# Performance work log

Measured on AMD Instinct MI355X. Metric: run time of the kernel, lower is better.

## Reference

```python
import jax, jax.numpy as jnp
import numpy as np

N = 50000        # n nodes (cells)
C = 1024         # common genes
H = 128          # edge_h_dim
HG = 128         # edge_hidden
E = 1600000      # edges (avg degree 32)
LAYERS = 2       # gnn_layers (unset in original __init__; fixed here)
EPS = 1e-8


def setup_inputs() -> dict:
    key = jax.random.key(0)
    ks = jax.random.split(key, 10)
    x_common = jax.random.normal(ks[0], (N, C), dtype=jnp.float32)
    src = jax.random.randint(ks[1], (E,), 0, N, dtype=jnp.int32)
    dst = jax.random.randint(ks[2], (E,), 0, N, dtype=jnp.int32)
    base_w = jax.random.uniform(ks[3], (E,), dtype=jnp.float32)
    # encoder params: Linear(C,H) -> ReLU -> Linear(H,H) -> ReLU
    W1 = jax.random.normal(ks[4], (C, H), dtype=jnp.float32) * 0.02
    b1 = jnp.zeros((H,), dtype=jnp.float32)
    W2 = jax.random.normal(ks[5], (H, H), dtype=jnp.float32) * 0.1
    b2 = jnp.zeros((H,), dtype=jnp.float32)
    # edge gate params: Linear(2H, HG) -> ReLU -> Linear(HG, 1)
    Wg1 = jax.random.normal(ks[6], (2 * H, HG), dtype=jnp.float32) * 0.1
    bg1 = jnp.zeros((HG,), dtype=jnp.float32)
    Wg2 = jax.random.normal(ks[7], (HG, 1), dtype=jnp.float32) * 0.1
    bg2 = jnp.full((1,), 2.0, dtype=jnp.float32)  # original init: bias=2.0
    # node reliability logits
    rho_raw = jax.random.normal(ks[8], (N,), dtype=jnp.float32) * 0.5
    return dict(x_common=x_common, src=src, dst=dst, base_w=base_w,
                W1=W1, b1=b1, W2=W2, b2=b2,
                Wg1=Wg1, bg1=bg1, Wg2=Wg2, bg2=bg2, rho_raw=rho_raw)


def reference(x_common, src, dst, base_w, W1, b1, W2, b2, Wg1, bg1, Wg2, bg2, rho_raw):
    # enc: [N, C] -> [N, H]
    h = jax.nn.relu(jax.nn.relu(x_common @ W1 + b1) @ W2 + b2)
    rho = jax.nn.sigmoid(rho_raw)                 # [N]
    rr = rho[src] * rho[dst]                      # [E] per-edge reliability factor
    for _ in range(LAYERS):
        h_src = h[src]                            # [E, H] gather
        h_dst = h[dst]                            # [E, H] gather
        z = jnp.concatenate([h_src, h_dst], axis=1)               # [E, 2H]
        gate = jax.nn.sigmoid(jax.nn.relu(z @ Wg1 + bg1) @ Wg2 + bg2)[:, 0]  # [E]
        w = base_w * gate * rr                    # [E]
        m = jax.ops.segment_sum(w[:, None] * h_src, dst, num_segments=N)     # [N, H]
        deg = jax.ops.segment_sum(w, dst, num_segments=N)                    # [N]
        h = m / (deg[:, None] + EPS)
    return h
```

## Files before the change

### kernel.cpp

```cpp
#include <hip/hip_runtime.h>
#include <stdint.h>

#define NN 50000
#define CC 1024
#define HH 128
#define EE 1600000
#define EPSV 1e-8f
#define NSTRIPE 8
#define STRIPE_N 6250
#define NBUCK (NN*NSTRIPE)
#define SCAN_BLKS 1563

typedef __attribute__((ext_vector_type(8))) short bf16x8;
typedef __attribute__((ext_vector_type(4))) float f32x4;
typedef __attribute__((ext_vector_type(2))) float f32x2;

__device__ __forceinline__ unsigned short f32_to_bf16(float f){
  union { float f; uint32_t u; } cv; cv.f = f;
  uint32_t u = cv.u;
  return (unsigned short)((u + 0x7FFFu + ((u >> 16) & 1u)) >> 16);
}
__device__ __forceinline__ float bf16lo_to_f32(uint32_t w){
  union { uint32_t u; float f; } cv; cv.u = w << 16; return cv.f;
}
__device__ __forceinline__ float bf16hi_to_f32(uint32_t w){
  union { uint32_t u; float f; } cv; cv.u = w & 0xFFFF0000u; return cv.f;
}

#define DPP_ADD(x, ctrl) ((x) + __int_as_float(__builtin_amdgcn_update_dpp(0, __float_as_int(x), (ctrl), 0xF, 0xF, true)))

#define GLOAD_LDS16(g, l) __builtin_amdgcn_global_load_lds( \
    (const __attribute__((address_space(1))) uint32_t*)(g), \
    (__attribute__((address_space(3))) uint32_t*)(l), 16, 0, 0)


__global__ __launch_bounds__(256) void k_prep_all(
    const float* __restrict__ W1, const float* __restrict__ W2,
    const float* __restrict__ Wg1,
    unsigned short* __restrict__ W1T, unsigned short* __restrict__ W2T,
    unsigned short* __restrict__ Wg1T){
  int idx = blockIdx.x*256 + threadIdx.x;
  if(idx < 131072){
    int n = idx >> 10, k = idx & 1023;
    W1T[idx] = f32_to_bf16(W1[k*128 + n]);
  } else if(idx < 131072 + 16384){
    int i = idx - 131072;
    int n = i >> 7, k = i & 127;
    W2T[i] = f32_to_bf16(W2[k*128 + n]);
  } else if(idx < 131072 + 16384 + 32768){
    int i = idx - 131072 - 16384;
    int c = i >> 7, k = i & 127;
    int row = (c < 128) ? k : (128 + k);
    int col = (c < 128) ? c : (c - 128);
    Wg1T[i] = f32_to_bf16(Wg1[row*128 + col]);
  }
}


__global__ __launch_bounds__(256) void k_hist(const int* __restrict__ src,
    const int* __restrict__ dst, int* __restrict__ counts,
    int* __restrict__ rank){
  int e = blockIdx.x*256 + threadIdx.x;
  if(e >= EE) return;
  int key = dst[e]*NSTRIPE + (int)((unsigned)src[e] / STRIPE_N);
  rank[e] = atomicAdd(&counts[key], 1);
}

__global__ __launch_bounds__(256) void k_scan1(const int* __restrict__ counts,
    int* __restrict__ lexcl, int* __restrict__ bsum){
  __shared__ int buf[256];
  const int t = threadIdx.x, i = blockIdx.x*256 + t;
  int v = (i < NBUCK) ? counts[i] : 0;
  buf[t] = v;
  __syncthreads();
  for(int off = 1; off < 256; off <<= 1){
    int add = (t >= off) ? buf[t-off] : 0;
    __syncthreads();
    buf[t] += add;
    __syncthreads();
  }
  if(i < NBUCK) lexcl[i] = buf[t] - v;
  if(t == 255) bsum[blockIdx.x] = buf[255];
}

__global__ __launch_bounds__(1024) void k_scan_mid(const int* __restrict__ bsum,
    int* __restrict__ bexcl){
  __shared__ int buf[1024];
  __shared__ int carry_s;
  const int t = threadIdx.x;
  if(t == 0) carry_s = 0;
  __syncthreads();
  for(int base = 0; base < SCAN_BLKS; base += 1024){
    int v = (base+t < SCAN_BLKS) ? bsum[base+t] : 0;
    buf[t] = v;
    __syncthreads();
    for(int off = 1; off < 1024; off <<= 1){
      int add = (t >= off) ? buf[t-off] : 0;
      __syncthreads();
      buf[t] += add;
      __syncthreads();
    }
    int carry = carry_s;
    if(base+t < SCAN_BLKS) bexcl[base+t] = carry + buf[t] - v;
    __syncthreads();
    if(t == 1023) carry_s = carry + buf[1023];
    __syncthreads();
  }
}

__global__ __launch_bounds__(256) void k_scan3(const int* __restrict__ lexcl,
    const int* __restrict__ bexcl, int* __restrict__ bptr){
  const int i = blockIdx.x*256 + threadIdx.x;
  if(i < NBUCK) bptr[i] = lexcl[i] + bexcl[blockIdx.x];
  if(i == 0) bptr[NBUCK] = EE;
}

__global__ __launch_bounds__(256) void k_fill(const int* __restrict__ src,
    const int* __restrict__ dst, const float* __restrict__ base_w,
    const float* __restrict__ rho_raw, const int* __restrict__ bptr,
    const int* __restrict__ rank, float2* __restrict__ scp){
  int e = blockIdx.x*256 + threadIdx.x;
  if(e >= EE) return;
  int s = src[e], d = dst[e];
  int key = d*NSTRIPE + (int)((unsigned)s / STRIPE_N);
  int p = bptr[key] + rank[e];
  float rs = 1.f/(1.f + __expf(-rho_raw[s]));
  float rd = 1.f/(1.f + __expf(-rho_raw[d]));
  scp[p] = make_float2(base_w[e]*rs*rd, __int_as_float(s));
}


__global__ __launch_bounds__(256) void k_enc1(
    const float* __restrict__ X, const unsigned short* __restrict__ W1T,
    const float* __restrict__ b1, unsigned short* __restrict__ h1)
{
  __shared__ __attribute__((aligned(16))) float          Af[3][32*32];
  __shared__ __attribute__((aligned(16))) unsigned short Bf[3][128*32];

  const int t = threadIdx.x, w = t >> 6, lane = t & 63;
  const int rowL = lane & 15, kq = lane >> 4;
  const int wm = w >> 1, wn = w & 1;
  const int row0 = blockIdx.x * 32;

  const int a_rl = w*8 + (lane >> 3);
  const int a_cl = lane & 7;
  int agr = row0 + a_rl; if(agr >= NN) agr = NN-1;
  const float* a_src = X + (size_t)agr*1024 + (a_cl ^ (a_rl & 7))*4;
  const int b_rl0 = w*32 + (lane >> 2);
  const int b_cl  = lane & 3;
  const int bkey0 = (b_rl0 ^ (b_rl0 >> 2)) & 3;
  const int bkey1 = ((b_rl0+16) ^ ((b_rl0+16) >> 2)) & 3;
  const unsigned short* b_src0 = W1T + (size_t)b_rl0*1024 + (b_cl ^ bkey0)*8;
  const unsigned short* b_src1 = W1T + (size_t)(b_rl0+16)*1024 + (b_cl ^ bkey1)*8;

  #define STAGE(buf, k0)  do{                                              \
    GLOAD_LDS16(a_src  + (k0), &Af[buf][(w*8)*32]);                        \
    GLOAD_LDS16(b_src0 + (k0), &Bf[buf][(w*32     )*32]);                  \
    GLOAD_LDS16(b_src1 + (k0), &Bf[buf][(w*32 + 16)*32]);                  \
  }while(0)

  f32x4 acc[4] = {};
  const int arow  = wm*16 + rowL;
  const int akey  = rowL & 7;
  const int bkeyR = (rowL ^ (rowL >> 2)) & 3;

  auto COMPUTE = [&](const float* afb, const unsigned short* bfb){
    f32x4 x0 = *(const f32x4*)&afb[arow*32 + (((2*kq  ) ^ akey) << 2)];
    f32x4 x1 = *(const f32x4*)&afb[arow*32 + (((2*kq+1) ^ akey) << 2)];
    union { bf16x8 v; unsigned short s[8]; } pk;
    #pragma unroll
    for(int j = 0; j < 4; j++){ pk.s[j] = f32_to_bf16(x0[j]); pk.s[4+j] = f32_to_bf16(x1[j]); }
    bf16x8 bfr[4];
    #pragma unroll
    for(int nf = 0; nf < 4; nf++){
      const int br = wn*64 + nf*16 + rowL;
      bfr[nf] = *(const bf16x8*)&bfb[br*32 + ((kq ^ bkeyR) << 3)];
    }
    #pragma unroll
    for(int nf = 0; nf < 4; nf++)
      acc[nf] = __builtin_amdgcn_mfma_f32_16x16x32_bf16(pk.v, bfr[nf], acc[nf], 0, 0, 0);
  };

  #define STEP(cbuf, sbuf, sk, vN)  do{                                    \
    if((sk) >= 0) STAGE(sbuf, (sk)*32);                                    \
    asm volatile("s_waitcnt vmcnt(" #vN ")" ::: "memory");                 \
    __builtin_amdgcn_s_barrier();                                          \
    __builtin_amdgcn_sched_barrier(0);                                     \
    COMPUTE(&Af[cbuf][0], &Bf[cbuf][0]);                                   \
    __builtin_amdgcn_s_barrier();                                          \
  }while(0)

  STAGE(0, 0);
  STAGE(1, 32);

  for(int tt = 0; tt < 30; tt += 3){
    STEP(0, 2, tt + 2, 6);
    STEP(1, 0, tt + 3, 6);
    STEP(2, 1, tt + 4, 6);
  }
  STEP(0, 0, -1, 3);
  asm volatile("s_waitcnt vmcnt(0)" ::: "memory");
  __builtin_amdgcn_s_barrier();
  __builtin_amdgcn_sched_barrier(0);
  COMPUTE(&Af[1][0], &Bf[1][0]);
  #undef STEP
  #undef STAGE

  #pragma unroll
  for(int nf = 0; nf < 4; nf++){
    const int col = wn*64 + nf*16 + rowL;
    const float bv = b1[col];
    #pragma unroll
    for(int r = 0; r < 4; r++){
      const int gr = row0 + wm*16 + kq*4 + r;
      if(gr < NN) h1[(size_t)gr*128 + col] = f32_to_bf16(fmaxf(acc[nf][r] + bv, 0.f));
    }
  }
}


__device__ __forceinline__ void uv_phase2(
    const unsigned short* hs, const unsigned short* wgl, int row0, int wave, int lane,
    const float* __restrict__ bg1,
    unsigned short* __restrict__ UH, float* __restrict__ Vf)
{
  const int rowL = lane & 15, kq = lane >> 4;
  const int r = wave*16 + rowL;
  f32x4 acc[16] = {};
  #pragma unroll
  for(int ks = 0; ks < 4; ks++){
    const int kc = ks*4 + kq;
    bf16x8 a = *(const bf16x8*)&hs[r*128 + ((kc ^ (r & 15)) << 3)];
    #pragma unroll
    for(int nt = 0; nt < 16; nt++){
      bf16x8 b = *(const bf16x8*)&wgl[(nt*16 + rowL)*128 + ((kc ^ rowL) << 3)];
      acc[nt] = __builtin_amdgcn_mfma_f32_16x16x32_bf16(a, b, acc[nt], 0, 0, 0);
    }
  }
  #pragma unroll
  for(int nt = 0; nt < 16; nt++){
    const int col = nt*16 + rowL;
    #pragma unroll
    for(int rr = 0; rr < 4; rr++){
      const int gr = row0 + wave*16 + kq*4 + rr;
      if(gr < NN){
        if(col < 128) UH[(size_t)gr*256 + col] = f32_to_bf16(acc[nt][rr]);
        else          Vf[(size_t)gr*128 + col - 128] = acc[nt][rr] + bg1[col - 128];
      }
    }
  }
}


__global__ __launch_bounds__(256) void k_uvA(
    const unsigned short* __restrict__ h1, const unsigned short* __restrict__ W2T,
    const float* __restrict__ b2, const unsigned short* __restrict__ Wg1T,
    const float* __restrict__ bg1, unsigned short* __restrict__ UH,
    float* __restrict__ Vf)
{
  __shared__ __attribute__((aligned(16))) unsigned short hs[64*128];
  __shared__ __attribute__((aligned(16))) unsigned short wgl[256*128];
  const int t = threadIdx.x, wave = t >> 6, lane = t & 63;
  const int rowL = lane & 15, kq = lane >> 4;
  const int row0 = blockIdx.x*64;

  bf16x8 wreg[16];
  #pragma unroll
  for(int i = 0; i < 16; i++)
    wreg[i] = *(const bf16x8*)(Wg1T + (i*256 + t)*8);

  int ar = row0 + wave*16 + rowL; if(ar >= NN) ar = NN-1;
  f32x4 acc[8] = {};
  #pragma unroll
  for(int ks = 0; ks < 4; ks++){
    bf16x8 a = *(const bf16x8*)(h1 + (size_t)ar*128 + ks*32 + kq*8);
    #pragma unroll
    for(int nt = 0; nt < 8; nt++){
      bf16x8 b = *(const bf16x8*)(W2T + (nt*16 + rowL)*128 + ks*32 + kq*8);
      acc[nt] = __builtin_amdgcn_mfma_f32_16x16x32_bf16(a, b, acc[nt], 0, 0, 0);
    }
  }
  #pragma unroll
  for(int nt = 0; nt < 8; nt++){
    const int col = nt*16 + rowL;
    const float bv = b2[col];
    #pragma unroll
    for(int r = 0; r < 4; r++){
      const int rw = wave*16 + kq*4 + r;
      const unsigned short hv = f32_to_bf16(fmaxf(acc[nt][r] + bv, 0.f));
      hs[rw*128 + (((col >> 3) ^ (rw & 15)) << 3) + (col & 7)] = hv;
    }
  }
  #pragma unroll
  for(int i = 0; i < 16; i++){
    const int idx = i*256 + t, row = idx >> 4, c = idx & 15;
    *(bf16x8*)&wgl[row*128 + ((c ^ (row & 15)) << 3)] = wreg[i];
  }
  __syncthreads();
  {
    const int r = t >> 2, gr = row0 + r;
    if(gr < NN){
      #pragma unroll
      for(int j8 = 0; j8 < 4; j8++){
        const int chunk = (t & 3)*4 + j8;
        bf16x8 v = *(const bf16x8*)&hs[r*128 + ((chunk ^ (r & 15)) << 3)];
        *(bf16x8*)&UH[(size_t)gr*256 + 128 + chunk*8] = v;
      }
    }
  }
  uv_phase2(hs, wgl, row0, wave, lane, bg1, UH, Vf);
}


__global__ __launch_bounds__(256) void k_uvB(
    const float* __restrict__ hf, const unsigned short* __restrict__ Wg1T,
    const float* __restrict__ bg1, unsigned short* __restrict__ UH,
    float* __restrict__ Vf)
{
  __shared__ __attribute__((aligned(16))) unsigned short hs[64*128];
  __shared__ __attribute__((aligned(16))) unsigned short wgl[256*128];
  const int t = threadIdx.x, wave = t >> 6, lane = t & 63;
  const int row0 = blockIdx.x*64;

  bf16x8 wreg[16];
  #pragma unroll
  for(int i = 0; i < 16; i++)
    wreg[i] = *(const bf16x8*)(Wg1T + (i*256 + t)*8);

  {
    const int r = t >> 2, gr0 = row0 + r;
    const int gr = (gr0 < NN) ? gr0 : NN-1;
    const float* p = hf + (size_t)gr*128 + (t & 3)*32;
    #pragma unroll
    for(int j8 = 0; j8 < 4; j8++){
      f32x4 v0 = *(const f32x4*)(p + j8*8);
      f32x4 v1 = *(const f32x4*)(p + j8*8 + 4);
      union { bf16x8 v; unsigned short s[8]; } pk;
      #pragma unroll
      for(int j = 0; j < 4; j++){ pk.s[j] = f32_to_bf16(v0[j]); pk.s[4+j] = f32_to_bf16(v1[j]); }
      const int chunk = (t & 3)*4 + j8;
      *(bf16x8*)&hs[r*128 + ((chunk ^ (r & 15)) << 3)] = pk.v;
      if(gr0 < NN) *(bf16x8*)&UH[(size_t)gr0*256 + 128 + chunk*8] = pk.v;
    }
  }
  #pragma unroll
  for(int i = 0; i < 16; i++){
    const int idx = i*256 + t, row = idx >> 4, c = idx & 15;
    *(bf16x8*)&wgl[row*128 + ((c ^ (row & 15)) << 3)] = wreg[i];
  }
  __syncthreads();
  uv_phase2(hs, wgl, row0, wave, lane & 63, bg1, UH, Vf);
}


__global__ __launch_bounds__(256) void k_gate_agg(
    const unsigned short* __restrict__ UH, const float* __restrict__ Vf,
    const int* __restrict__ bptr, const float2* __restrict__ scp,
    const float* __restrict__ Wg2, const float* __restrict__ bg2p,
    float* __restrict__ out_f32)
{
  __shared__ float2 ws_s[4][64];
  const int wv = threadIdx.x >> 6, lane = threadIdx.x & 63;
  const int gw = blockIdx.x*4 + wv;
  if(gw >= NN) return;
  const int eq = lane >> 4, li = lane & 15;

  f32x4 va = *(const f32x4*)(Vf + (size_t)gw*128 + li*8);
  f32x4 vb = *(const f32x4*)(Vf + (size_t)gw*128 + li*8 + 4);
  f32x4 wa = *(const f32x4*)(Wg2 + li*8);
  f32x4 wb = *(const f32x4*)(Wg2 + li*8 + 4);
  const float vch[8]  = {va[0],va[1],va[2],va[3],vb[0],vb[1],vb[2],vb[3]};
  const float w2ch[8] = {wa[0],wa[1],wa[2],wa[3],wb[0],wb[1],wb[2],wb[3]};
  const float bg2v = bg2p[0];

  const int beg = bptr[gw*NSTRIPE], end = bptr[gw*NSTRIPE + NSTRIPE];
  float a0 = 0.f, a1 = 0.f, wsum = 0.f;

  for(int base = beg; base < end; base += 64){
    const int nb = min(64, end - base);

    float2 sc_c0, sc_c1; bf16x8 u_c0, u_c1;
    {
      const int i0 = (eq     < nb) ? eq     : 0;
      const int i1 = (4 + eq < nb) ? 4 + eq : 0;
      sc_c0 = scp[base + i0]; sc_c1 = scp[base + i1];
      u_c0 = *(const bf16x8*)&UH[(uint32_t)__float_as_int(sc_c0.y)*256u + li*8];
      u_c1 = *(const bf16x8*)&UH[(uint32_t)__float_as_int(sc_c1.y)*256u + li*8];
    }
    for(int q = 0; q < nb; q += 8){
      float2 sc_n0 = sc_c0, sc_n1 = sc_c1; bf16x8 u_n0 = u_c0, u_n1 = u_c1;
      if(q + 8 < nb){
        const int i0 = (q + 8  + eq < nb) ? q + 8  + eq : 0;
        const int i1 = (q + 12 + eq < nb) ? q + 12 + eq : 0;
        sc_n0 = scp[base + i0]; sc_n1 = scp[base + i1];
        u_n0 = *(const bf16x8*)&UH[(uint32_t)__float_as_int(sc_n0.y)*256u + li*8];
        u_n1 = *(const bf16x8*)&UH[(uint32_t)__float_as_int(sc_n1.y)*256u + li*8];
      }
      {
        union { bf16x8 v; uint32_t u32[4]; } uu; uu.v = u_c0;
        float tacc = 0.f;
        #pragma unroll
        for(int p = 0; p < 4; p++){
          const uint32_t w2b = uu.u32[p];
          tacc += fmaxf(bf16lo_to_f32(w2b) + vch[2*p],   0.f) * w2ch[2*p];
          tacc += fmaxf(bf16hi_to_f32(w2b) + vch[2*p+1], 0.f) * w2ch[2*p+1];
        }
        tacc = DPP_ADD(tacc, 0xB1);
        tacc = DPP_ADD(tacc, 0x4E);
        tacc = DPP_ADD(tacc, 0x141);
        tacc = DPP_ADD(tacc, 0x140);
        const float g = 1.f/(1.f + __expf(-(tacc + bg2v)));
        const int idx = q + eq;
        if(li == 0 && idx < nb) ws_s[wv][idx] = make_float2(sc_c0.x*g, sc_c0.y);
      }
      {
        union { bf16x8 v; uint32_t u32[4]; } uu; uu.v = u_c1;
        float tacc = 0.f;
        #pragma unroll
        for(int p = 0; p < 4; p++){
          const uint32_t w2b = uu.u32[p];
          tacc += fmaxf(bf16lo_to_f32(w2b) + vch[2*p],   0.f) * w2ch[2*p];
          tacc += fmaxf(bf16hi_to_f32(w2b) + vch[2*p+1], 0.f) * w2ch[2*p+1];
        }
        tacc = DPP_ADD(tacc, 0xB1);
        tacc = DPP_ADD(tacc, 0x4E);
        tacc = DPP_ADD(tacc, 0x141);
        tacc = DPP_ADD(tacc, 0x140);
        const float g = 1.f/(1.f + __expf(-(tacc + bg2v)));
        const int idx = q + 4 + eq;
        if(li == 0 && idx < nb) ws_s[wv][idx] = make_float2(sc_c1.x*g, sc_c1.y);
      }
      sc_c0 = sc_n0; sc_c1 = sc_n1; u_c0 = u_n0; u_c1 = u_n1;
    }

    #pragma unroll 8
    for(int j = 0; j < nb; j++){
      const float2 p = ws_s[wv][j];
      const float w  = p.x;
      const uint32_t s = (uint32_t)__float_as_int(p.y);
      const uint32_t hw = *(const uint32_t*)&UH[s*256u + 128u + lane*2];
      a0 += w*bf16lo_to_f32(hw);
      a1 += w*bf16hi_to_f32(hw);
      wsum += w;
    }
  }
  const float inv = 1.f/(wsum + EPSV);
  const size_t o = (size_t)gw*128 + lane*2;
  *(f32x2*)&out_f32[o] = (f32x2){a0*inv, a1*inv};
}


extern "C" void kernel_launch(void* const* d_in, const int* in_sizes, int n_in,
                              void* d_out, int out_size, void* d_ws, size_t ws_size,
                              hipStream_t stream) {
  (void)in_sizes; (void)n_in; (void)out_size; (void)ws_size;
  const float* X      = (const float*)d_in[0];
  const int*   src    = (const int*)d_in[1];
  const int*   dst    = (const int*)d_in[2];
  const float* base_w = (const float*)d_in[3];
  const float* W1     = (const float*)d_in[4];
  const float* b1     = (const float*)d_in[5];
  const float* W2     = (const float*)d_in[6];
  const float* b2     = (const float*)d_in[7];
  const float* Wg1    = (const float*)d_in[8];
  const float* bg1    = (const float*)d_in[9];
  const float* Wg2    = (const float*)d_in[10];
  const float* bg2    = (const float*)d_in[11];
  const float* rho    = (const float*)d_in[12];

  char* ws = (char*)d_ws;
  size_t off = 0;
  auto alloc = [&](size_t bytes)->char*{ char* p = ws + off; off += (bytes + 255) & ~(size_t)255; return p; };
  unsigned short* W1T      = (unsigned short*)alloc((size_t)1024*128*2);
  unsigned short* W2T      = (unsigned short*)alloc((size_t)128*128*2);
  unsigned short* Wg1T     = (unsigned short*)alloc((size_t)256*128*2);
  int*            rank     = (int*)alloc((size_t)EE*4);
  float2*         scp      = (float2*)alloc((size_t)EE*8);
  int*            bptr     = (int*)alloc((size_t)(NBUCK+1)*4);
  int*            counts   = (int*)alloc((size_t)NBUCK*4);
  int*            lexcl    = (int*)alloc((size_t)NBUCK*4);
  int*            bsum     = (int*)alloc((size_t)SCAN_BLKS*4);
  int*            bexcl    = (int*)alloc((size_t)SCAN_BLKS*4);
  unsigned short* h1       = (unsigned short*)alloc((size_t)NN*128*2);
  unsigned short* UH       = (unsigned short*)alloc((size_t)NN*256*2);
  float*          Vf       = (float*)alloc((size_t)NN*128*4);
  float*          hf_B     = (float*)alloc((size_t)NN*128*4);

  hipMemsetAsync(counts, 0, (size_t)NBUCK*4, stream);
  k_prep_all<<<704, 256, 0, stream>>>(W1, W2, Wg1, W1T, W2T, Wg1T);
  k_hist<<<EE/256, 256, 0, stream>>>(src, dst, counts, rank);
  k_scan1<<<SCAN_BLKS, 256, 0, stream>>>(counts, lexcl, bsum);
  k_scan_mid<<<1, 1024, 0, stream>>>(bsum, bexcl);
  k_scan3<<<SCAN_BLKS, 256, 0, stream>>>(lexcl, bexcl, bptr);
  k_fill<<<EE/256, 256, 0, stream>>>(src, dst, base_w, rho, bptr, rank, scp);

  k_enc1<<<1563, 256, 0, stream>>>(X, W1T, b1, h1);

  k_uvA<<<782, 256, 0, stream>>>(h1, W2T, b2, Wg1T, bg1, UH, Vf);
  k_gate_agg<<<12500, 256, 0, stream>>>(UH, Vf, bptr, scp, Wg2, bg2, hf_B);
  k_uvB<<<782, 256, 0, stream>>>(hf_B, Wg1T, bg1, UH, Vf);
  k_gate_agg<<<12500, 256, 0, stream>>>(UH, Vf, bptr, scp, Wg2, bg2, (float*)d_out);
}
```

Measured before the change: 510.0 us.

## Double k_enc1 row tile to 64 and switch to double-buffered pipeline

```diff
diff --git a/kernel.cpp b/kernel.cpp
--- a/kernel.cpp
+++ b/kernel.cpp
@@ -134,18 +134,20 @@
     const float* __restrict__ X, const unsigned short* __restrict__ W1T,
     const float* __restrict__ b1, unsigned short* __restrict__ h1)
 {
-  __shared__ __attribute__((aligned(16))) float          Af[3][32*32];
-  __shared__ __attribute__((aligned(16))) unsigned short Bf[3][128*32];
+  __shared__ __attribute__((aligned(16))) float          Af[2][64*32];
+  __shared__ __attribute__((aligned(16))) unsigned short Bf[2][128*32];
 
   const int t = threadIdx.x, w = t >> 6, lane = t & 63;
   const int rowL = lane & 15, kq = lane >> 4;
   const int wm = w >> 1, wn = w & 1;
-  const int row0 = blockIdx.x * 32;
-
-  const int a_rl = w*8 + (lane >> 3);
-  const int a_cl = lane & 7;
-  int agr = row0 + a_rl; if(agr >= NN) agr = NN-1;
-  const float* a_src = X + (size_t)agr*1024 + (a_cl ^ (a_rl & 7))*4;
+  const int row0 = blockIdx.x * 64;
+
+  const int a_rl0 = w*16 + (lane >> 3);
+  const int a_cl  = lane & 7;
+  int agr0 = row0 + a_rl0;     if(agr0 >= NN) agr0 = NN-1;
+  int agr1 = row0 + a_rl0 + 8; if(agr1 >= NN) agr1 = NN-1;
+  const float* a_src0 = X + (size_t)agr0*1024 + (a_cl ^ (a_rl0 & 7))*4;
+  const float* a_src1 = X + (size_t)agr1*1024 + (a_cl ^ ((a_rl0+8) & 7))*4;
   const int b_rl0 = w*32 + (lane >> 2);
   const int b_cl  = lane & 3;
   const int bkey0 = (b_rl0 ^ (b_rl0 >> 2)) & 3;
@@ -154,22 +156,29 @@
   const unsigned short* b_src1 = W1T + (size_t)(b_rl0+16)*1024 + (b_cl ^ bkey1)*8;
 
   #define STAGE(buf, k0)  do{                                              \
-    GLOAD_LDS16(a_src  + (k0), &Af[buf][(w*8)*32]);                        \
+    GLOAD_LDS16(a_src0 + (k0), &Af[buf][(w*16    )*32]);                   \
+    GLOAD_LDS16(a_src1 + (k0), &Af[buf][(w*16 + 8)*32]);                   \
     GLOAD_LDS16(b_src0 + (k0), &Bf[buf][(w*32     )*32]);                  \
     GLOAD_LDS16(b_src1 + (k0), &Bf[buf][(w*32 + 16)*32]);                  \
   }while(0)
 
-  f32x4 acc[4] = {};
-  const int arow  = wm*16 + rowL;
+  f32x4 acc[2][4] = {};
+  const int arow0 = wm*32 + rowL;
   const int akey  = rowL & 7;
   const int bkeyR = (rowL ^ (rowL >> 2)) & 3;
 
   auto COMPUTE = [&](const float* afb, const unsigned short* bfb){
-    f32x4 x0 = *(const f32x4*)&afb[arow*32 + (((2*kq  ) ^ akey) << 2)];
-    f32x4 x1 = *(const f32x4*)&afb[arow*32 + (((2*kq+1) ^ akey) << 2)];
-    union { bf16x8 v; unsigned short s[8]; } pk;
-    #pragma unroll
-    for(int j = 0; j < 4; j++){ pk.s[j] = f32_to_bf16(x0[j]); pk.s[4+j] = f32_to_bf16(x1[j]); }
+    bf16x8 af[2];
+    #pragma unroll
+    for(int mf = 0; mf < 2; mf++){
+      const int ar = arow0 + mf*16;
+      f32x4 x0 = *(const f32x4*)&afb[ar*32 + (((2*kq  ) ^ akey) << 2)];
+      f32x4 x1 = *(const f32x4*)&afb[ar*32 + (((2*kq+1) ^ akey) << 2)];
+      union { bf16x8 v; unsigned short s[8]; } pk;
+      #pragma unroll
+      for(int j = 0; j < 4; j++){ pk.s[j] = f32_to_bf16(x0[j]); pk.s[4+j] = f32_to_bf16(x1[j]); }
+      af[mf] = pk.v;
+    }
     bf16x8 bfr[4];
     #pragma unroll
     for(int nf = 0; nf < 4; nf++){
@@ -177,13 +186,15 @@
       bfr[nf] = *(const bf16x8*)&bfb[br*32 + ((kq ^ bkeyR) << 3)];
     }
     #pragma unroll
-    for(int nf = 0; nf < 4; nf++)
-      acc[nf] = __builtin_amdgcn_mfma_f32_16x16x32_bf16(pk.v, bfr[nf], acc[nf], 0, 0, 0);
+    for(int mf = 0; mf < 2; mf++)
+      #pragma unroll
+      for(int nf = 0; nf < 4; nf++)
+        acc[mf][nf] = __builtin_amdgcn_mfma_f32_16x16x32_bf16(af[mf], bfr[nf], acc[mf][nf], 0, 0, 0);
   };
 
-  #define STEP(cbuf, sbuf, sk, vN)  do{                                    \
-    if((sk) >= 0) STAGE(sbuf, (sk)*32);                                    \
-    asm volatile("s_waitcnt vmcnt(" #vN ")" ::: "memory");                 \
+  #define STEP(cbuf, sbuf, sk)  do{                                        \
+    STAGE(sbuf, (sk)*32);                                                  \
+    asm volatile("s_waitcnt vmcnt(4)" ::: "memory");                       \
     __builtin_amdgcn_s_barrier();                                          \
     __builtin_amdgcn_sched_barrier(0);                                     \
     COMPUTE(&Af[cbuf][0], &Bf[cbuf][0]);                                   \
@@ -191,14 +202,11 @@
   }while(0)
 
   STAGE(0, 0);
-  STAGE(1, 32);
-
-  for(int tt = 0; tt < 30; tt += 3){
-    STEP(0, 2, tt + 2, 6);
-    STEP(1, 0, tt + 3, 6);
-    STEP(2, 1, tt + 4, 6);
-  }
-  STEP(0, 0, -1, 3);
+  for(int tt = 0; tt < 30; tt += 2){
+    STEP(0, 1, tt + 1);
+    STEP(1, 0, tt + 2);
+  }
+  STEP(0, 1, 31);
   asm volatile("s_waitcnt vmcnt(0)" ::: "memory");
   __builtin_amdgcn_s_barrier();
   __builtin_amdgcn_sched_barrier(0);
@@ -207,13 +215,16 @@
   #undef STAGE
 
   #pragma unroll
-  for(int nf = 0; nf < 4; nf++){
-    const int col = wn*64 + nf*16 + rowL;
-    const float bv = b1[col];
-    #pragma unroll
-    for(int r = 0; r < 4; r++){
-      const int gr = row0 + wm*16 + kq*4 + r;
-      if(gr < NN) h1[(size_t)gr*128 + col] = f32_to_bf16(fmaxf(acc[nf][r] + bv, 0.f));
+  for(int mf = 0; mf < 2; mf++){
+    #pragma unroll
+    for(int nf = 0; nf < 4; nf++){
+      const int col = wn*64 + nf*16 + rowL;
+      const float bv = b1[col];
+      #pragma unroll
+      for(int r = 0; r < 4; r++){
+        const int gr = row0 + wm*32 + mf*16 + kq*4 + r;
+        if(gr < NN) h1[(size_t)gr*128 + col] = f32_to_bf16(fmaxf(acc[mf][nf][r] + bv, 0.f));
+      }
     }
   }
 }
@@ -494,7 +505,7 @@
   k_scan3<<<SCAN_BLKS, 256, 0, stream>>>(lexcl, bexcl, bptr);
   k_fill<<<EE/256, 256, 0, stream>>>(src, dst, base_w, rho, bptr, rank, scp);
 
-  k_enc1<<<1563, 256, 0, stream>>>(X, W1T, b1, h1);
+  k_enc1<<<782, 256, 0, stream>>>(X, W1T, b1, h1);
 
   k_uvA<<<782, 256, 0, stream>>>(h1, W2T, b2, Wg1T, bg1, UH, Vf);
   k_gate_agg<<<12500, 256, 0, stream>>>(UH, Vf, bptr, scp, Wg2, bg2, hf_B);
```

New measurement: 498.7 us. -2.2%, faster.
